# Performance work log

Measured on AMD Instinct MI355X. Metric: run time of the kernel, lower is better.

## Reference

```python
import jax, jax.numpy as jnp
import numpy as np

THETA = 10000.0
BLOCK_SIZE = 8192  # max_cache_len; T >= BLOCK_SIZE triggers eviction
NEG_INF = -1e30


def _rope_cos_sin(head_dim, seq_len, dtype):
    inv_freq = 1.0 / (THETA ** (jnp.arange(0, head_dim, 2, dtype=jnp.float32) / head_dim))
    freqs = jnp.arange(seq_len, dtype=jnp.float32)[:, None] * inv_freq[None, :]  # (T, hd/2)
    return jnp.cos(freqs).astype(dtype), jnp.sin(freqs).astype(dtype)


def _apply_rope(x, cos, sin):
    # x: (B, T, hd); complex multiply on interleaved pairs, matching torch.view_as_complex
    B, T, hd = x.shape
    xr = x.reshape(B, T, hd // 2, 2)
    x0, x1 = xr[..., 0], xr[..., 1]
    out = jnp.stack([x0 * cos - x1 * sin, x0 * sin + x1 * cos], axis=-1)
    return out.reshape(B, T, hd)


def setup_inputs() -> dict:
    key = jax.random.key(0)
    kx, kk, kq, kv = jax.random.split(key, 4)
    B, T, C, hd = 1, 8192, 1024, 64
    x = jax.random.normal(kx, (B, T, C), dtype=jnp.float32)
    Wk = 0.02 * jax.random.normal(kk, (C, hd), dtype=jnp.float32)
    Wq = 0.02 * jax.random.normal(kq, (C, hd), dtype=jnp.float32)
    Wv = 0.02 * jax.random.normal(kv, (C, hd), dtype=jnp.float32)
    return {"x": x, "Wk": Wk, "Wq": Wq, "Wv": Wv}


def reference(x, Wk, Wq, Wv):
    # Warm-up branch of Head.forward: RoPE QK causal attention + importance-based eviction.
    B, T, C = x.shape
    hd = Wk.shape[1]
    k = x @ Wk  # (B, T, hd)
    q = x @ Wq
    v = x @ Wv
    cos, sin = _rope_cos_sin(hd, T, x.dtype)
    k = _apply_rope(k, cos, sin)
    q = _apply_rope(q, cos, sin)
    scale = hd ** -0.5
    scores = jnp.einsum('btd,bsd->bts', q, k) * scale  # (B, T, T)
    causal = jnp.tril(jnp.ones((T, T), dtype=bool))
    scores = jnp.where(causal[None], scores, NEG_INF)
    wei = jax.nn.softmax(scores, axis=-1)
    out = jnp.einsum('bts,bsd->btd', wei, v)  # (B, T, hd)
    # importance-based KV-cache eviction (T >= BLOCK_SIZE here)
    col_sums = wei.sum(axis=1)  # (B, T)
    evict_id = jnp.argmin(col_sums.reshape(-1))  # flattened argmin, as torch.argmin (B=1)
    keep = jnp.arange(T - 1)
    keep = keep + (keep >= evict_id)  # all indices except evict_id
    importance = jnp.take(wei, keep, axis=1)  # evict row in dim 1: (B, T-1, T)
    cache_k = jnp.take(k, keep, axis=1)       # (B, T-1, hd)
    cache_v = jnp.take(v, keep, axis=1)       # (B, T-1, hd)
    return out, importance, cache_k, cache_v
```

## Files before the change

kernel.cpp:

```cpp
#include <hip/hip_runtime.h>

#define TT 8192
#define CC 1024
#define HD 64
#define TAIL0 (TT - 64)
#define IMP_OFF ((size_t)TT * HD)
#define CK_OFF (IMP_OFF + (size_t)(TT - 1) * TT)
#define CV_OFF (CK_OFF + (size_t)(TT - 1) * HD)

typedef float f32x4 __attribute__((ext_vector_type(4)));
typedef short short8 __attribute__((ext_vector_type(8)));

static __device__ __forceinline__ short f2bf(float f) {
  union { float f; unsigned u; } v; v.f = f;
  unsigned u = v.u;
  unsigned r = (u + 0x7fffu + ((u >> 16) & 1u)) >> 16;
  return (short)r;
}
static __device__ __forceinline__ float bf2f(short h) {
  union { unsigned u; float f; } v;
  v.u = ((unsigned)(unsigned short)h) << 16;
  return v.f;
}
static __device__ __forceinline__ f32x4 mfma16(short8 a, short8 b, f32x4 c) {
  return __builtin_amdgcn_mfma_f32_16x16x32_bf16(a, b, c, 0, 0, 0);
}

__global__ void prep(const float* __restrict__ Wk, const float* __restrict__ Wq,
                     const float* __restrict__ Wv, short* __restrict__ wth,
                     short* __restrict__ wtl, float* __restrict__ colsums,
                     float* __restrict__ ctab, float* __restrict__ stab) {
  const int b = blockIdx.x;
  if (b < 768) {
    const int tid = b * 256 + threadIdx.x;
    const int col = tid >> 10, c = tid & 1023;
    const int m = col >> 6, d = col & 63;
    const float* W = (m == 0) ? Wk : (m == 1) ? Wq : Wv;
    const float w = W[c * HD + d];
    const short h = f2bf(w);
    wth[col * CC + c] = h;
    wtl[col * CC + c] = f2bf(w - bf2f(h));
  } else if (b < 800) {
    const int t = (b - 768) * 256 + threadIdx.x;
    colsums[t] = 0.0f;
  } else {
    const int t = (b - 800) * 256 + threadIdx.x;
    const int row = t >> 5, fi = t & 31;
    const float inv = (float)(1.0 / pow(10000.0, (double)fi / 32.0));
    const float ang = (float)row * inv;
    float sn, cs;
    sincosf(ang, &sn, &cs);
    ctab[t] = cs; stab[t] = sn;
  }
}

__global__ __launch_bounds__(256) void qkv_rope(
    const float* __restrict__ x, const short* __restrict__ wth,
    const short* __restrict__ wtl, const float* __restrict__ ctab,
    const float* __restrict__ stab,
    short* __restrict__ qb, short* __restrict__ kb, short* __restrict__ vt,
    float* __restrict__ kf, float* __restrict__ vf, float* __restrict__ qf) {
  __shared__ short xsh[16][1024];
  __shared__ short xsl[16][1024];
  const int tid = threadIdx.x;
  const int lane = tid & 63, wv = tid >> 6;
  const int g = lane >> 4, lr = lane & 15, g8 = g * 8;
  const int r0 = blockIdx.x * 16;

  for (int i = tid; i < 16 * 128; i += 256) {
    const int row = i >> 7, u = i & 127;
    const float4 a4 = *(const float4*)&x[(size_t)(r0 + row) * CC + u * 8];
    const float4 b4 = *(const float4*)&x[(size_t)(r0 + row) * CC + u * 8 + 4];
    const float xv[8] = {a4.x, a4.y, a4.z, a4.w, b4.x, b4.y, b4.z, b4.w};
    short8 h, l;
#pragma unroll
    for (int t = 0; t < 8; ++t) {
      h[t] = f2bf(xv[t]);
      l[t] = f2bf(xv[t] - bf2f(h[t]));
    }
    const int us = (u ^ (row & 7)) * 8;
    *(short8*)&xsh[row][us] = h;
    *(short8*)&xsl[row][us] = l;
  }
  __syncthreads();

  const int ct0 = wv * 3;
  f32x4 acc[3];
#pragma unroll
  for (int i = 0; i < 3; ++i) acc[i] = (f32x4){0.f, 0.f, 0.f, 0.f};
  for (int kc = 0; kc < 32; ++kc) {
    const int us = ((kc * 4 + g) ^ (lr & 7)) * 8;
    const short8 ah = *(const short8*)&xsh[lr][us];
    const short8 al = *(const short8*)&xsl[lr][us];
    const int k0 = kc * 32 + g8;
#pragma unroll
    for (int t = 0; t < 3; ++t) {
      const int ct = ct0 + t;
      const short8 bh = *(const short8*)&wth[(ct * 16 + lr) * CC + k0];
      const short8 bl = *(const short8*)&wtl[(ct * 16 + lr) * CC + k0];
      acc[t] = mfma16(ah, bh, acc[t]);
      acc[t] = mfma16(al, bh, acc[t]);
      acc[t] = mfma16(ah, bl, acc[t]);
    }
  }
#pragma unroll
  for (int t = 0; t < 3; ++t) {
    const int col = ct0 * 16 + t * 16 + lr;
    const int m = col >> 6, d = col & 63;
#pragma unroll
    for (int r = 0; r < 4; ++r) {
      const int row = r0 + g * 4 + r;
      const float val = acc[t][r];
      if (m == 2) {
        vf[row * HD + d] = val;
        vt[(size_t)d * TT + row] = f2bf(val);
      } else {
        const float partner = __shfl_xor(val, 1);
        const int fi = d >> 1;
        const float cs = ctab[row * 32 + fi];
        const float sn = stab[row * 32 + fi];
        const float res = (d & 1) ? (partner * sn + val * cs)
                                  : (val * cs - partner * sn);
        if (m == 0) { kf[row * HD + d] = res; kb[row * HD + d] = f2bf(res); }
        else        { qf[row * HD + d] = res; qb[row * HD + d] = f2bf(res); }
      }
    }
  }
}

__global__ __launch_bounds__(512) void attn_row(
    const short* __restrict__ qb, const short* __restrict__ kb,
    const short* __restrict__ vt, float* __restrict__ colsums,
    float* __restrict__ outp, float* __restrict__ stash,
    float* __restrict__ linv_g) {
  const int tid = threadIdx.x;
  const int lane = tid & 63, wv = tid >> 6;
  const int g = lane >> 4, lr = lane & 15, g8 = g * 8;
  const int bid = (int)blockIdx.x;
  const int rt = (bid < 256) ? (511 - bid) : (bid - 256);
  const int r0 = rt * 16, rmax = r0 + 15;
  const int nkt = rt + 1;
  const int nktp = (nkt + 1) >> 1;
  float* imp = outp + IMP_OFF;
  const float4 z4 = (float4){0.f, 0.f, 0.f, 0.f};

  __shared__ float et[8][16][36];
  __shared__ float l4[8][16];

  const short8 a0 = *(const short8*)&qb[(r0 + lr) * HD + g8];
  const short8 a1 = *(const short8*)&qb[(r0 + lr) * HD + 32 + g8];

  float lacc[4] = {0.f, 0.f, 0.f, 0.f};
  for (int kt = wv; kt < nkt; kt += 8) {
    const int j0 = kt * 16;
    const short8 b0 = *(const short8*)&kb[(j0 + lr) * HD + g8];
    const short8 b1 = *(const short8*)&kb[(j0 + lr) * HD + 32 + g8];
    f32x4 sv = (f32x4){0.f, 0.f, 0.f, 0.f};
    sv = mfma16(a0, b0, sv);
    sv = mfma16(a1, b1, sv);
    const int j = j0 + lr;
#pragma unroll
    for (int r = 0; r < 4; ++r) {
      const int i = r0 + g * 4 + r;
      if (j <= i) lacc[r] += __expf(sv[r] * 0.125f);
    }
  }
#pragma unroll
  for (int r = 0; r < 4; ++r) {
#pragma unroll
    for (int m = 1; m < 16; m <<= 1) lacc[r] += __shfl_xor(lacc[r], m);
  }
  if (lr == 0) {
#pragma unroll
    for (int r = 0; r < 4; ++r) l4[wv][g * 4 + r] = lacc[r];
  }
  __syncthreads();
  float rinv[4];
#pragma unroll
  for (int r = 0; r < 4; ++r) {
    const int row = g * 4 + r;
    float s = 0.f;
#pragma unroll
    for (int w = 0; w < 8; ++w) s += l4[w][row];
    rinv[r] = 1.0f / s;
  }
  if (wv == 0 && lr == 0) {
#pragma unroll
    for (int r = 0; r < 4; ++r) linv_g[r0 + g * 4 + r] = rinv[r];
  }

  f32x4 oacc[4];
#pragma unroll
  for (int ct = 0; ct < 4; ++ct) oacc[ct] = (f32x4){0.f, 0.f, 0.f, 0.f};
  const int worow = lane >> 3, wof4 = (lane & 7) * 4;
  for (int kp = wv; kp < nktp; kp += 8) {
    const int j0p = kp * 32;
#pragma unroll
    for (int h = 0; h < 2; ++h) {
      const int j0 = j0p + h * 16;
      float w4[4] = {0.f, 0.f, 0.f, 0.f};
      if (j0 <= rmax) {
        const short8 b0 = *(const short8*)&kb[(j0 + lr) * HD + g8];
        const short8 b1 = *(const short8*)&kb[(j0 + lr) * HD + 32 + g8];
        f32x4 sv = (f32x4){0.f, 0.f, 0.f, 0.f};
        sv = mfma16(a0, b0, sv);
        sv = mfma16(a1, b1, sv);
        const int j = j0 + lr;
#pragma unroll
        for (int r = 0; r < 4; ++r) {
          const int i = r0 + g * 4 + r;
          w4[r] = (j <= i) ? __expf(sv[r] * 0.125f) * rinv[r] : 0.0f;
        }
        float csum = w4[0] + w4[1] + w4[2] + w4[3];
        csum += __shfl_xor(csum, 16);
        csum += __shfl_xor(csum, 32);
        if (lane < 16 && csum > 0.f) atomicAdd(&colsums[j0 + lane], csum);
      }
#pragma unroll
      for (int r = 0; r < 4; ++r) et[wv][g * 4 + r][h * 16 + lr] = w4[r];
    }
    const float4 e0 = *(const float4*)&et[wv][lr][g8];
    const float4 e1 = *(const float4*)&et[wv][lr][g8 + 4];
    short8 ea;
    ea[0] = f2bf(e0.x); ea[1] = f2bf(e0.y); ea[2] = f2bf(e0.z); ea[3] = f2bf(e0.w);
    ea[4] = f2bf(e1.x); ea[5] = f2bf(e1.y); ea[6] = f2bf(e1.z); ea[7] = f2bf(e1.w);
#pragma unroll
    for (int ct = 0; ct < 4; ++ct) {
      const short8 bv = *(const short8*)&vt[(size_t)(ct * 16 + lr) * TT + j0p + g8];
      oacc[ct] = mfma16(ea, bv, oacc[ct]);
    }
#pragma unroll
    for (int p = 0; p < 2; ++p) {
      const int row = p * 8 + worow;
      const int i = r0 + row;
      const float4 v = *(const float4*)&et[wv][row][wof4];
      if (i < TT - 1) *(float4*)&imp[(size_t)i * TT + j0p + wof4] = v;
      else            *(float4*)&stash[j0p + wof4] = v;
    }
  }
  const int zstart = nktp * 32;
  for (int row = 0; row < 16; ++row) {
    const int i = r0 + row;
    float* dst = (i < TT - 1) ? &imp[(size_t)i * TT] : stash;
    for (int c = zstart + tid * 4; c < TT; c += 2048) *(float4*)&dst[c] = z4;
  }
  __syncthreads();
  float* cbuf = &et[0][0][0];
#pragma unroll
  for (int step = 4; step >= 1; step >>= 1) {
    if (wv >= step && wv < 2 * step) {
      float* dst = cbuf + (size_t)(wv - step) * 1024;
#pragma unroll
      for (int ct = 0; ct < 4; ++ct)
#pragma unroll
        for (int r = 0; r < 4; ++r)
          dst[(g * 4 + r) * 64 + ct * 16 + lr] = oacc[ct][r];
    }
    __syncthreads();
    if (wv < step) {
      const float* src = cbuf + (size_t)wv * 1024;
#pragma unroll
      for (int ct = 0; ct < 4; ++ct)
#pragma unroll
        for (int r = 0; r < 4; ++r)
          oacc[ct][r] += src[(g * 4 + r) * 64 + ct * 16 + lr];
    }
    __syncthreads();
  }
  if (wv == 0) {
#pragma unroll
    for (int ct = 0; ct < 4; ++ct)
#pragma unroll
      for (int r = 0; r < 4; ++r)
        outp[(size_t)(r0 + g * 4 + r) * HD + ct * 16 + lr] = oacc[ct][r];
  }
}

__global__ __launch_bounds__(256) void tail_exact(
    const float* __restrict__ qf, const float* __restrict__ kf,
    float* __restrict__ l_exact, float* __restrict__ tail_e) {
  const int b = blockIdx.x;
  const int i = TAIL0 + b;
  const int tid = threadIdx.x;
  __shared__ float qs[64];
  __shared__ float ws4[4];
  if (tid < 64) {
    qs[tid] = qf[i * HD + tid];
    if (TAIL0 + tid > i) tail_e[(b << 6) + tid] = 0.0f;
  }
  __syncthreads();
  float part = 0.f;
  for (int j = tid; j <= i; j += 256) {
    const float* kr = &kf[(size_t)j * HD];
    float dot = 0.f;
#pragma unroll
    for (int d = 0; d < 64; ++d) dot += qs[d] * kr[d];
    const float e = expf(dot * 0.125f);
    part += e;
    if (j >= TAIL0) tail_e[(b << 6) + (j - TAIL0)] = e;
  }
#pragma unroll
  for (int m = 1; m < 64; m <<= 1) part += __shfl_xor(part, m);
  if ((tid & 63) == 0) ws4[tid >> 6] = part;
  __syncthreads();
  if (tid == 0) l_exact[b] = ws4[0] + ws4[1] + ws4[2] + ws4[3];
}

__global__ void argmin_k(const float* __restrict__ colsums,
                         const float* __restrict__ l_exact,
                         const float* __restrict__ tail_e,
                         int* __restrict__ evict) {
  __shared__ float sv[4];
  __shared__ int si[4];
  const int tid = threadIdx.x, lane = tid & 63, wv = tid >> 6;
  float best = 3.4e38f; int bi = TT;
  for (int j = tid; j < TT; j += 256) {
    float v;
    if (j >= TAIL0) {
      const int jc = j - TAIL0;
      v = 0.f;
      for (int b = jc; b < 64; ++b) v += tail_e[(b << 6) + jc] / l_exact[b];
    } else {
      v = colsums[j];
    }
    if (v < best) { best = v; bi = j; }
  }
#pragma unroll
  for (int m = 1; m < 64; m <<= 1) {
    const float ov = __shfl_xor(best, m);
    const int oi = __shfl_xor(bi, m);
    if (ov < best || (ov == best && oi < bi)) { best = ov; bi = oi; }
  }
  if (lane == 0) { sv[wv] = best; si[wv] = bi; }
  __syncthreads();
  if (tid == 0) {
    for (int w = 1; w < 4; ++w)
      if (sv[w] < best || (sv[w] == best && si[w] < bi)) { best = sv[w]; bi = si[w]; }
    evict[0] = bi;
  }
}

__global__ __launch_bounds__(256) void fix_cache(
    const float* __restrict__ qf, const float* __restrict__ kf,
    const float* __restrict__ vf, const float* __restrict__ linv,
    const float* __restrict__ stash, const int* __restrict__ evict,
    float* __restrict__ outp) {
  const int bid = (int)blockIdx.x;
  const int tid = threadIdx.x;
  const int eid = evict[0];
  if (bid < 512) {
    float* imp = outp + IMP_OFF;
    __shared__ float qs[64];
    for (int dst = eid + bid; dst < TT - 1; dst += 512) {
      const int src = dst + 1;
      if (src == TT - 1) {
        for (int c = tid; c < TT / 4; c += 256)
          ((float4*)&imp[(size_t)dst * TT])[c] = ((const float4*)stash)[c];
      } else {
        if (tid < 64) qs[tid] = qf[src * HD + tid];
        __syncthreads();
        const float rinv = linv[src];
        for (int j = tid; j < TT; j += 256) {
          float w = 0.f;
          if (j <= src) {
            const float* kr = &kf[(size_t)j * HD];
            float dot = 0.f;
#pragma unroll
            for (int d = 0; d < 64; ++d) dot += qs[d] * kr[d];
            w = expf(dot * 0.125f) * rinv;
          }
          imp[(size_t)dst * TT + j] = w;
        }
        __syncthreads();
      }
    }
  } else {
    const int t = (bid - 512) * 256 + tid;
    const int per = (TT - 1) * (HD / 4);
    if (t >= 2 * per) return;
    const int m = t / per;
    const int rem = t - m * per;
    const int r = rem >> 4, c4 = rem & 15;
    const int src = r + (r >= eid);
    const float* sp = m ? vf : kf;
    const float4 val = *(const float4*)&sp[src * HD + c4 * 4];
    float* dst = outp + (m ? CV_OFF : CK_OFF);
    *(float4*)&dst[r * HD + c4 * 4] = val;
  }
}

extern "C" void kernel_launch(void* const* d_in, const int* in_sizes, int n_in,
                              void* d_out, int out_size, void* d_ws, size_t ws_size,
                              hipStream_t stream) {
  const float* x  = (const float*)d_in[0];
  const float* Wk = (const float*)d_in[1];
  const float* Wq = (const float*)d_in[2];
  const float* Wv = (const float*)d_in[3];
  float* outp = (float*)d_out;
  char* ws = (char*)d_ws;
  short* qb      = (short*)(ws);
  short* kb      = (short*)(ws + (1u << 20));
  short* vt      = (short*)(ws + (2u << 20));
  float* kf      = (float*)(ws + (3u << 20));
  float* vf      = (float*)(ws + (5u << 20));
  float* qf      = (float*)(ws + (7u << 20));
  float* linv    = (float*)(ws + (9u << 20));
  int*   evict   = (int*)  (ws + (9u << 20) + (64u << 10));
  float* colsums = (float*)(ws + (9u << 20) + (384u << 10));
  short* wth     = (short*)(ws + (9u << 20) + (448u << 10));
  short* wtl     = (short*)(ws + (9u << 20) + (832u << 10));
  float* tail_e  = (float*)(ws + (9u << 20) + (1280u << 10));
  float* l_exact = (float*)(ws + (9u << 20) + (1344u << 10));
  float* stash   = (float*)(ws + (9u << 20) + (1408u << 10));
  float* ctab    = (float*)(ws + (12u << 20));
  float* stab    = (float*)(ws + (13u << 20));

  prep<<<1824, 256, 0, stream>>>(Wk, Wq, Wv, wth, wtl, colsums, ctab, stab);
  qkv_rope<<<512, 256, 0, stream>>>(x, wth, wtl, ctab, stab, qb, kb, vt, kf, vf, qf);
  attn_row<<<512, 512, 0, stream>>>(qb, kb, vt, colsums, outp, stash, linv);
  tail_exact<<<64, 256, 0, stream>>>(qf, kf, l_exact, tail_e);
  argmin_k<<<1, 256, 0, stream>>>(colsums, l_exact, tail_e, evict);
  fix_cache<<<1536, 256, 0, stream>>>(qf, kf, vf, linv, stash, evict, outp);
}
```

Baseline: 280.4 us.

## Unroll attention loops by two tiles and use nontemporal stores for importance output

The row-sum and weight/PV loops in attn_row now process two key tiles per iteration. Loads for both are issued up front, and the second tile goes into separate LDS staging and accumulators, so more memory-level parallelism hides load latency. The large importance matrix writes, the zero fill, and the cache copies switch to nontemporal stores to avoid polluting cache with write-once data. The cost is extra LDS (a second staging buffer) and higher register pressure, which may reduce occupancy.

Result: faster. 264.2 us (-5.8%).

```diff
diff --git a/kernel.cpp b/kernel.cpp
--- a/kernel.cpp
+++ b/kernel.cpp
@@ -24,6 +24,9 @@
 }
 static __device__ __forceinline__ f32x4 mfma16(short8 a, short8 b, f32x4 c) {
   return __builtin_amdgcn_mfma_f32_16x16x32_bf16(a, b, c, 0, 0, 0);
+}
+static __device__ __forceinline__ void nt_store4(float* p, f32x4 v) {
+  __builtin_nontemporal_store(v, (f32x4*)p);
 }
 
 __global__ void prep(const float* __restrict__ Wk, const float* __restrict__ Wq,
@@ -142,27 +145,41 @@
   const int nkt = rt + 1;
   const int nktp = (nkt + 1) >> 1;
   float* imp = outp + IMP_OFF;
-  const float4 z4 = (float4){0.f, 0.f, 0.f, 0.f};
+  const f32x4 z4 = (f32x4){0.f, 0.f, 0.f, 0.f};
 
   __shared__ float et[8][16][36];
+  __shared__ float et2[8][16][36];
   __shared__ float l4[8][16];
 
   const short8 a0 = *(const short8*)&qb[(r0 + lr) * HD + g8];
   const short8 a1 = *(const short8*)&qb[(r0 + lr) * HD + 32 + g8];
 
   float lacc[4] = {0.f, 0.f, 0.f, 0.f};
-  for (int kt = wv; kt < nkt; kt += 8) {
-    const int j0 = kt * 16;
-    const short8 b0 = *(const short8*)&kb[(j0 + lr) * HD + g8];
-    const short8 b1 = *(const short8*)&kb[(j0 + lr) * HD + 32 + g8];
-    f32x4 sv = (f32x4){0.f, 0.f, 0.f, 0.f};
-    sv = mfma16(a0, b0, sv);
-    sv = mfma16(a1, b1, sv);
-    const int j = j0 + lr;
+  for (int kt = wv; kt < nkt; kt += 16) {
+    const int ktb = kt + 8;
+    const bool has1 = (ktb < nkt);
+    const int j00 = kt * 16, j01 = ktb * 16;
+    const short8 b00 = *(const short8*)&kb[(j00 + lr) * HD + g8];
+    const short8 b01 = *(const short8*)&kb[(j00 + lr) * HD + 32 + g8];
+    short8 b10, b11;
+    if (has1) {
+      b10 = *(const short8*)&kb[(j01 + lr) * HD + g8];
+      b11 = *(const short8*)&kb[(j01 + lr) * HD + 32 + g8];
+    }
+    f32x4 sv0 = z4;
+    sv0 = mfma16(a0, b00, sv0);
+    sv0 = mfma16(a1, b01, sv0);
+    f32x4 sv1 = z4;
+    if (has1) {
+      sv1 = mfma16(a0, b10, sv1);
+      sv1 = mfma16(a1, b11, sv1);
+    }
+    const int jj0 = j00 + lr, jj1 = j01 + lr;
 #pragma unroll
     for (int r = 0; r < 4; ++r) {
       const int i = r0 + g * 4 + r;
-      if (j <= i) lacc[r] += __expf(sv[r] * 0.125f);
+      if (jj0 <= i) lacc[r] += __expf(sv0[r] * 0.125f);
+      if (has1 && jj1 <= i) lacc[r] += __expf(sv1[r] * 0.125f);
     }
   }
 #pragma unroll
@@ -189,61 +206,99 @@
     for (int r = 0; r < 4; ++r) linv_g[r0 + g * 4 + r] = rinv[r];
   }
 
-  f32x4 oacc[4];
-#pragma unroll
-  for (int ct = 0; ct < 4; ++ct) oacc[ct] = (f32x4){0.f, 0.f, 0.f, 0.f};
+  f32x4 oacc[4], oacc2[4];
+#pragma unroll
+  for (int ct = 0; ct < 4; ++ct) { oacc[ct] = z4; oacc2[ct] = z4; }
   const int worow = lane >> 3, wof4 = (lane & 7) * 4;
-  for (int kp = wv; kp < nktp; kp += 8) {
-    const int j0p = kp * 32;
-#pragma unroll
-    for (int h = 0; h < 2; ++h) {
-      const int j0 = j0p + h * 16;
-      float w4[4] = {0.f, 0.f, 0.f, 0.f};
-      if (j0 <= rmax) {
-        const short8 b0 = *(const short8*)&kb[(j0 + lr) * HD + g8];
-        const short8 b1 = *(const short8*)&kb[(j0 + lr) * HD + 32 + g8];
-        f32x4 sv = (f32x4){0.f, 0.f, 0.f, 0.f};
-        sv = mfma16(a0, b0, sv);
-        sv = mfma16(a1, b1, sv);
-        const int j = j0 + lr;
-#pragma unroll
-        for (int r = 0; r < 4; ++r) {
-          const int i = r0 + g * 4 + r;
-          w4[r] = (j <= i) ? __expf(sv[r] * 0.125f) * rinv[r] : 0.0f;
+  for (int kp = wv; kp < nktp; kp += 16) {
+    const int kpb = kp + 8;
+    const bool has1 = (kpb < nktp);
+    const int j0p0 = kp * 32, j0p1 = kpb * 32;
+    short8 bv0[4], bv1[4];
+#pragma unroll
+    for (int ct = 0; ct < 4; ++ct)
+      bv0[ct] = *(const short8*)&vt[(size_t)(ct * 16 + lr) * TT + j0p0 + g8];
+    if (has1) {
+#pragma unroll
+      for (int ct = 0; ct < 4; ++ct)
+        bv1[ct] = *(const short8*)&vt[(size_t)(ct * 16 + lr) * TT + j0p1 + g8];
+    }
+#pragma unroll
+    for (int c = 0; c < 2; ++c) {
+      if (c == 1 && !has1) break;
+      const int j0p = c ? j0p1 : j0p0;
+      float (*etp)[36] = c ? et2[wv] : et[wv];
+#pragma unroll
+      for (int h = 0; h < 2; ++h) {
+        const int j0 = j0p + h * 16;
+        float w4[4] = {0.f, 0.f, 0.f, 0.f};
+        if (j0 <= rmax) {
+          const short8 b0 = *(const short8*)&kb[(j0 + lr) * HD + g8];
+          const short8 b1 = *(const short8*)&kb[(j0 + lr) * HD + 32 + g8];
+          f32x4 sv = z4;
+          sv = mfma16(a0, b0, sv);
+          sv = mfma16(a1, b1, sv);
+          const int j = j0 + lr;
+#pragma unroll
+          for (int r = 0; r < 4; ++r) {
+            const int i = r0 + g * 4 + r;
+            w4[r] = (j <= i) ? __expf(sv[r] * 0.125f) * rinv[r] : 0.0f;
+          }
+          float csum = w4[0] + w4[1] + w4[2] + w4[3];
+          csum += __shfl_xor(csum, 16);
+          csum += __shfl_xor(csum, 32);
+          if (lane < 16 && csum > 0.f) atomicAdd(&colsums[j0 + lane], csum);
         }
-        float csum = w4[0] + w4[1] + w4[2] + w4[3];
-        csum += __shfl_xor(csum, 16);
-        csum += __shfl_xor(csum, 32);
-        if (lane < 16 && csum > 0.f) atomicAdd(&colsums[j0 + lane], csum);
+#pragma unroll
+        for (int r = 0; r < 4; ++r) etp[g * 4 + r][h * 16 + lr] = w4[r];
       }
-#pragma unroll
-      for (int r = 0; r < 4; ++r) et[wv][g * 4 + r][h * 16 + lr] = w4[r];
-    }
-    const float4 e0 = *(const float4*)&et[wv][lr][g8];
-    const float4 e1 = *(const float4*)&et[wv][lr][g8 + 4];
-    short8 ea;
-    ea[0] = f2bf(e0.x); ea[1] = f2bf(e0.y); ea[2] = f2bf(e0.z); ea[3] = f2bf(e0.w);
-    ea[4] = f2bf(e1.x); ea[5] = f2bf(e1.y); ea[6] = f2bf(e1.z); ea[7] = f2bf(e1.w);
-#pragma unroll
-    for (int ct = 0; ct < 4; ++ct) {
-      const short8 bv = *(const short8*)&vt[(size_t)(ct * 16 + lr) * TT + j0p + g8];
-      oacc[ct] = mfma16(ea, bv, oacc[ct]);
+    }
+    {
+      const float4 e0 = *(const float4*)&et[wv][lr][g8];
+      const float4 e1 = *(const float4*)&et[wv][lr][g8 + 4];
+      short8 ea;
+      ea[0] = f2bf(e0.x); ea[1] = f2bf(e0.y); ea[2] = f2bf(e0.z); ea[3] = f2bf(e0.w);
+      ea[4] = f2bf(e1.x); ea[5] = f2bf(e1.y); ea[6] = f2bf(e1.z); ea[7] = f2bf(e1.w);
+#pragma unroll
+      for (int ct = 0; ct < 4; ++ct) oacc[ct] = mfma16(ea, bv0[ct], oacc[ct]);
+    }
+    if (has1) {
+      const float4 e0 = *(const float4*)&et2[wv][lr][g8];
+      const float4 e1 = *(const float4*)&et2[wv][lr][g8 + 4];
+      short8 ea;
+      ea[0] = f2bf(e0.x); ea[1] = f2bf(e0.y); ea[2] = f2bf(e0.z); ea[3] = f2bf(e0.w);
+      ea[4] = f2bf(e1.x); ea[5] = f2bf(e1.y); ea[6] = f2bf(e1.z); ea[7] = f2bf(e1.w);
+#pragma unroll
+      for (int ct = 0; ct < 4; ++ct) oacc2[ct] = mfma16(ea, bv1[ct], oacc2[ct]);
     }
 #pragma unroll
     for (int p = 0; p < 2; ++p) {
       const int row = p * 8 + worow;
       const int i = r0 + row;
-      const float4 v = *(const float4*)&et[wv][row][wof4];
-      if (i < TT - 1) *(float4*)&imp[(size_t)i * TT + j0p + wof4] = v;
-      else            *(float4*)&stash[j0p + wof4] = v;
+      const f32x4 v0 = *(const f32x4*)&et[wv][row][wof4];
+      if (i < TT - 1) nt_store4(&imp[(size_t)i * TT + j0p0 + wof4], v0);
+      else            *(f32x4*)&stash[j0p0 + wof4] = v0;
+      if (has1) {
+        const f32x4 v1 = *(const f32x4*)&et2[wv][row][wof4];
+        if (i < TT - 1) nt_store4(&imp[(size_t)i * TT + j0p1 + wof4], v1);
+        else            *(f32x4*)&stash[j0p1 + wof4] = v1;
+      }
     }
   }
   const int zstart = nktp * 32;
   for (int row = 0; row < 16; ++row) {
     const int i = r0 + row;
-    float* dst = (i < TT - 1) ? &imp[(size_t)i * TT] : stash;
-    for (int c = zstart + tid * 4; c < TT; c += 2048) *(float4*)&dst[c] = z4;
-  }
+    if (i < TT - 1) {
+      float* dst = &imp[(size_t)i * TT];
+      for (int c = zstart + tid * 4; c < TT; c += 2048) nt_store4(&dst[c], z4);
+    } else {
+      for (int c = zstart + tid * 4; c < TT; c += 2048) *(f32x4*)&stash[c] = z4;
+    }
+  }
+#pragma unroll
+  for (int ct = 0; ct < 4; ++ct)
+#pragma unroll
+    for (int r = 0; r < 4; ++r) oacc[ct][r] += oacc2[ct][r];
   __syncthreads();
   float* cbuf = &et[0][0][0];
 #pragma unroll
@@ -355,7 +410,7 @@
       const int src = dst + 1;
       if (src == TT - 1) {
         for (int c = tid; c < TT / 4; c += 256)
-          ((float4*)&imp[(size_t)dst * TT])[c] = ((const float4*)stash)[c];
+          ((f32x4*)&imp[(size_t)dst * TT])[c] = ((const f32x4*)stash)[c];
       } else {
         if (tid < 64) qs[tid] = qf[src * HD + tid];
         __syncthreads();
@@ -383,9 +438,9 @@
     const int r = rem >> 4, c4 = rem & 15;
     const int src = r + (r >= eid);
     const float* sp = m ? vf : kf;
-    const float4 val = *(const float4*)&sp[src * HD + c4 * 4];
+    const f32x4 val = *(const f32x4*)&sp[src * HD + c4 * 4];
     float* dst = outp + (m ? CV_OFF : CK_OFF);
-    *(float4*)&dst[r * HD + c4 * 4] = val;
+    nt_store4(&dst[r * HD + c4 * 4], val);
   }
 }
 
```

## Split attention into separate row-sum pass and two-way key-split weight pass

Applied to the files above, without the earlier changes.

Moves the softmax denominator computation out of the attention kernel into its own pass, parallelised over key chunks with single-wave blocks, plus a small reduction kernel that writes the inverse sums. The main attention kernel is then launched with a second grid dimension that splits the key range in two, accumulating the output rows with atomics into a buffer now zeroed in prep. The huge importance-matrix writes and the cache copies switch to nontemporal stores, and V-tile loads are hoisted ahead of the score MFMAs. This buys more parallelism and lower cache pollution at the cost of extra launches, recomputing QK scores twice, and atomic output accumulation.

After: 300.6 us. 1.07x slower.

```diff
diff --git a/kernel.cpp b/kernel.cpp
--- a/kernel.cpp
+++ b/kernel.cpp
@@ -25,11 +25,15 @@
 static __device__ __forceinline__ f32x4 mfma16(short8 a, short8 b, f32x4 c) {
   return __builtin_amdgcn_mfma_f32_16x16x32_bf16(a, b, c, 0, 0, 0);
 }
+static __device__ __forceinline__ void nt_store4(float* p, f32x4 v) {
+  __builtin_nontemporal_store(v, (f32x4*)p);
+}
 
 __global__ void prep(const float* __restrict__ Wk, const float* __restrict__ Wq,
                      const float* __restrict__ Wv, short* __restrict__ wth,
                      short* __restrict__ wtl, float* __restrict__ colsums,
-                     float* __restrict__ ctab, float* __restrict__ stab) {
+                     float* __restrict__ ctab, float* __restrict__ stab,
+                     float* __restrict__ outp) {
   const int b = blockIdx.x;
   if (b < 768) {
     const int tid = b * 256 + threadIdx.x;
@@ -43,7 +47,7 @@
   } else if (b < 800) {
     const int t = (b - 768) * 256 + threadIdx.x;
     colsums[t] = 0.0f;
-  } else {
+  } else if (b < 1824) {
     const int t = (b - 800) * 256 + threadIdx.x;
     const int row = t >> 5, fi = t & 31;
     const float inv = (float)(1.0 / pow(10000.0, (double)fi / 32.0));
@@ -51,6 +55,9 @@
     float sn, cs;
     sincosf(ang, &sn, &cs);
     ctab[t] = cs; stab[t] = sn;
+  } else {
+    const int t = (b - 1824) * 256 + threadIdx.x;
+    outp[t] = 0.0f;
   }
 }
 
@@ -128,31 +135,22 @@
   }
 }
 
-__global__ __launch_bounds__(512) void attn_row(
+__global__ __launch_bounds__(64) void lpass(
     const short* __restrict__ qb, const short* __restrict__ kb,
-    const short* __restrict__ vt, float* __restrict__ colsums,
-    float* __restrict__ outp, float* __restrict__ stash,
-    float* __restrict__ linv_g) {
-  const int tid = threadIdx.x;
-  const int lane = tid & 63, wv = tid >> 6;
+    float* __restrict__ l_part) {
+  const int lane = threadIdx.x & 63;
   const int g = lane >> 4, lr = lane & 15, g8 = g * 8;
-  const int bid = (int)blockIdx.x;
-  const int rt = (bid < 256) ? (511 - bid) : (bid - 256);
-  const int r0 = rt * 16, rmax = r0 + 15;
-  const int nkt = rt + 1;
-  const int nktp = (nkt + 1) >> 1;
-  float* imp = outp + IMP_OFF;
-  const float4 z4 = (float4){0.f, 0.f, 0.f, 0.f};
-
-  __shared__ float et[8][16][36];
-  __shared__ float l4[8][16];
-
+  const int rt = (int)gridDim.x - 1 - (int)blockIdx.x;
+  const int cc = blockIdx.y;
+  const int r0 = rt * 16, rmax = r0 + 15, c0 = cc * 1024;
+  float* lp = l_part + (size_t)cc * TT;
+  if (c0 > rmax) { if (lane < 16) lp[r0 + lane] = 0.0f; return; }
   const short8 a0 = *(const short8*)&qb[(r0 + lr) * HD + g8];
   const short8 a1 = *(const short8*)&qb[(r0 + lr) * HD + 32 + g8];
-
   float lacc[4] = {0.f, 0.f, 0.f, 0.f};
-  for (int kt = wv; kt < nkt; kt += 8) {
-    const int j0 = kt * 16;
+  const int nkt = min(64, (rmax - c0) / 16 + 1);
+  for (int kt = 0; kt < nkt; ++kt) {
+    const int j0 = c0 + kt * 16;
     const short8 b0 = *(const short8*)&kb[(j0 + lr) * HD + g8];
     const short8 b1 = *(const short8*)&kb[(j0 + lr) * HD + 32 + g8];
     f32x4 sv = (f32x4){0.f, 0.f, 0.f, 0.f};
@@ -172,29 +170,54 @@
   }
   if (lr == 0) {
 #pragma unroll
-    for (int r = 0; r < 4; ++r) l4[wv][g * 4 + r] = lacc[r];
-  }
-  __syncthreads();
+    for (int r = 0; r < 4; ++r) lp[r0 + g * 4 + r] = lacc[r];
+  }
+}
+
+__global__ void linv_k(const float* __restrict__ l_part, float* __restrict__ linv) {
+  const int i = blockIdx.x * 256 + threadIdx.x;
+  if (i >= TT) return;
+  float s = 0.f;
+#pragma unroll
+  for (int cc = 0; cc < 8; ++cc) s += l_part[(size_t)cc * TT + i];
+  linv[i] = 1.0f / s;
+}
+
+__global__ __launch_bounds__(512) void attn_b(
+    const short* __restrict__ qb, const short* __restrict__ kb,
+    const short* __restrict__ vt, const float* __restrict__ linv,
+    float* __restrict__ colsums, float* __restrict__ outp,
+    float* __restrict__ stash) {
+  const int tid = threadIdx.x;
+  const int lane = tid & 63, wv = tid >> 6;
+  const int g = lane >> 4, lr = lane & 15, g8 = g * 8;
+  const int bid = (int)blockIdx.x;
+  const int h2 = (int)blockIdx.y;
+  const int rt = (bid < 256) ? (511 - bid) : (bid - 256);
+  const int r0 = rt * 16, rmax = r0 + 15;
+  const int nkt = rt + 1;
+  const int nktp = (nkt + 1) >> 1;
+  float* imp = outp + IMP_OFF;
+  const f32x4 z4 = (f32x4){0.f, 0.f, 0.f, 0.f};
+
+  __shared__ float et[8][16][36];
+
+  const short8 a0 = *(const short8*)&qb[(r0 + lr) * HD + g8];
+  const short8 a1 = *(const short8*)&qb[(r0 + lr) * HD + 32 + g8];
   float rinv[4];
 #pragma unroll
-  for (int r = 0; r < 4; ++r) {
-    const int row = g * 4 + r;
-    float s = 0.f;
-#pragma unroll
-    for (int w = 0; w < 8; ++w) s += l4[w][row];
-    rinv[r] = 1.0f / s;
-  }
-  if (wv == 0 && lr == 0) {
-#pragma unroll
-    for (int r = 0; r < 4; ++r) linv_g[r0 + g * 4 + r] = rinv[r];
-  }
+  for (int r = 0; r < 4; ++r) rinv[r] = linv[r0 + g * 4 + r];
 
   f32x4 oacc[4];
 #pragma unroll
-  for (int ct = 0; ct < 4; ++ct) oacc[ct] = (f32x4){0.f, 0.f, 0.f, 0.f};
+  for (int ct = 0; ct < 4; ++ct) oacc[ct] = z4;
   const int worow = lane >> 3, wof4 = (lane & 7) * 4;
-  for (int kp = wv; kp < nktp; kp += 8) {
+  for (int kp = wv + 8 * h2; kp < nktp; kp += 16) {
     const int j0p = kp * 32;
+    short8 bv[4];
+#pragma unroll
+    for (int ct = 0; ct < 4; ++ct)
+      bv[ct] = *(const short8*)&vt[(size_t)(ct * 16 + lr) * TT + j0p + g8];
 #pragma unroll
     for (int h = 0; h < 2; ++h) {
       const int j0 = j0p + h * 16;
@@ -202,7 +225,7 @@
       if (j0 <= rmax) {
         const short8 b0 = *(const short8*)&kb[(j0 + lr) * HD + g8];
         const short8 b1 = *(const short8*)&kb[(j0 + lr) * HD + 32 + g8];
-        f32x4 sv = (f32x4){0.f, 0.f, 0.f, 0.f};
+        f32x4 sv = z4;
         sv = mfma16(a0, b0, sv);
         sv = mfma16(a1, b1, sv);
         const int j = j0 + lr;
@@ -225,24 +248,27 @@
     ea[0] = f2bf(e0.x); ea[1] = f2bf(e0.y); ea[2] = f2bf(e0.z); ea[3] = f2bf(e0.w);
     ea[4] = f2bf(e1.x); ea[5] = f2bf(e1.y); ea[6] = f2bf(e1.z); ea[7] = f2bf(e1.w);
 #pragma unroll
-    for (int ct = 0; ct < 4; ++ct) {
-      const short8 bv = *(const short8*)&vt[(size_t)(ct * 16 + lr) * TT + j0p + g8];
-      oacc[ct] = mfma16(ea, bv, oacc[ct]);
-    }
+    for (int ct = 0; ct < 4; ++ct) oacc[ct] = mfma16(ea, bv[ct], oacc[ct]);
 #pragma unroll
     for (int p = 0; p < 2; ++p) {
       const int row = p * 8 + worow;
       const int i = r0 + row;
-      const float4 v = *(const float4*)&et[wv][row][wof4];
-      if (i < TT - 1) *(float4*)&imp[(size_t)i * TT + j0p + wof4] = v;
-      else            *(float4*)&stash[j0p + wof4] = v;
+      const f32x4 v = *(const f32x4*)&et[wv][row][wof4];
+      if (i < TT - 1) nt_store4(&imp[(size_t)i * TT + j0p + wof4], v);
+      else            *(f32x4*)&stash[j0p + wof4] = v;
     }
   }
   const int zstart = nktp * 32;
   for (int row = 0; row < 16; ++row) {
     const int i = r0 + row;
-    float* dst = (i < TT - 1) ? &imp[(size_t)i * TT] : stash;
-    for (int c = zstart + tid * 4; c < TT; c += 2048) *(float4*)&dst[c] = z4;
+    if (i < TT - 1) {
+      float* dst = &imp[(size_t)i * TT];
+      for (int c = zstart + (tid + h2 * 512) * 4; c < TT; c += 4096)
+        nt_store4(&dst[c], z4);
+    } else {
+      for (int c = zstart + (tid + h2 * 512) * 4; c < TT; c += 4096)
+        *(f32x4*)&stash[c] = z4;
+    }
   }
   __syncthreads();
   float* cbuf = &et[0][0][0];
@@ -272,7 +298,7 @@
     for (int ct = 0; ct < 4; ++ct)
 #pragma unroll
       for (int r = 0; r < 4; ++r)
-        outp[(size_t)(r0 + g * 4 + r) * HD + ct * 16 + lr] = oacc[ct][r];
+        atomicAdd(&outp[(size_t)(r0 + g * 4 + r) * HD + ct * 16 + lr], oacc[ct][r]);
   }
 }
 
@@ -355,7 +381,7 @@
       const int src = dst + 1;
       if (src == TT - 1) {
         for (int c = tid; c < TT / 4; c += 256)
-          ((float4*)&imp[(size_t)dst * TT])[c] = ((const float4*)stash)[c];
+          ((f32x4*)&imp[(size_t)dst * TT])[c] = ((const f32x4*)stash)[c];
       } else {
         if (tid < 64) qs[tid] = qf[src * HD + tid];
         __syncthreads();
@@ -383,9 +409,9 @@
     const int r = rem >> 4, c4 = rem & 15;
     const int src = r + (r >= eid);
     const float* sp = m ? vf : kf;
-    const float4 val = *(const float4*)&sp[src * HD + c4 * 4];
+    const f32x4 val = *(const f32x4*)&sp[src * HD + c4 * 4];
     float* dst = outp + (m ? CV_OFF : CK_OFF);
-    *(float4*)&dst[r * HD + c4 * 4] = val;
+    nt_store4(&dst[r * HD + c4 * 4], val);
   }
 }
 
@@ -406,6 +432,7 @@
   float* qf      = (float*)(ws + (7u << 20));
   float* linv    = (float*)(ws + (9u << 20));
   int*   evict   = (int*)  (ws + (9u << 20) + (64u << 10));
+  float* l_part  = (float*)(ws + (9u << 20) + (128u << 10));
   float* colsums = (float*)(ws + (9u << 20) + (384u << 10));
   short* wth     = (short*)(ws + (9u << 20) + (448u << 10));
   short* wtl     = (short*)(ws + (9u << 20) + (832u << 10));
@@ -415,9 +442,11 @@
   float* ctab    = (float*)(ws + (12u << 20));
   float* stab    = (float*)(ws + (13u << 20));
 
-  prep<<<1824, 256, 0, stream>>>(Wk, Wq, Wv, wth, wtl, colsums, ctab, stab);
+  prep<<<3872, 256, 0, stream>>>(Wk, Wq, Wv, wth, wtl, colsums, ctab, stab, outp);
   qkv_rope<<<512, 256, 0, stream>>>(x, wth, wtl, ctab, stab, qb, kb, vt, kf, vf, qf);
-  attn_row<<<512, 512, 0, stream>>>(qb, kb, vt, colsums, outp, stash, linv);
+  lpass<<<dim3(512, 8), 64, 0, stream>>>(qb, kb, l_part);
+  linv_k<<<32, 256, 0, stream>>>(l_part, linv);
+  attn_b<<<dim3(512, 2), 512, 0, stream>>>(qb, kb, vt, linv, colsums, outp, stash);
   tail_exact<<<64, 256, 0, stream>>>(qf, kf, l_exact, tail_e);
   argmin_k<<<1, 256, 0, stream>>>(colsums, l_exact, tail_e, evict);
   fix_cache<<<1536, 256, 0, stream>>>(qf, kf, vf, linv, stash, evict, outp);
```

## Pre-swizzle K/V into MFMA fragment layout, double attn waves, nontemporal stores

Applied to the files above, without the earlier changes.

The QKV kernel now writes bf16 K and V in a layout that already matches the MFMA operand fragments, so each lane loads a contiguous short8 instead of doing strided row or transposed loads. The attention kernel grows from 8 to 16 waves per block, with larger shared reduction buffers and a deeper tree reduction. The large importance-matrix stores and the cache copies switch to nontemporal stores to cut cache pollution on the 256MB output write. The cost is more registers and shared memory per block, which may limit occupancy, and a scattered store pattern in qkv_rope.

Measured after the change: 230.3 us. 1.22x faster.

```diff
diff --git a/kernel.cpp b/kernel.cpp
--- a/kernel.cpp
+++ b/kernel.cpp
@@ -24,6 +24,9 @@
 }
 static __device__ __forceinline__ f32x4 mfma16(short8 a, short8 b, f32x4 c) {
   return __builtin_amdgcn_mfma_f32_16x16x32_bf16(a, b, c, 0, 0, 0);
+}
+static __device__ __forceinline__ void nt_store4(float* p, f32x4 v) {
+  __builtin_nontemporal_store(v, (f32x4*)p);
 }
 
 __global__ void prep(const float* __restrict__ Wk, const float* __restrict__ Wq,
@@ -58,7 +61,7 @@
     const float* __restrict__ x, const short* __restrict__ wth,
     const short* __restrict__ wtl, const float* __restrict__ ctab,
     const float* __restrict__ stab,
-    short* __restrict__ qb, short* __restrict__ kb, short* __restrict__ vt,
+    short* __restrict__ qb, short* __restrict__ kbb, short* __restrict__ vbb,
     float* __restrict__ kf, float* __restrict__ vf, float* __restrict__ qf) {
   __shared__ short xsh[16][1024];
   __shared__ short xsl[16][1024];
@@ -113,7 +116,10 @@
       const float val = acc[t][r];
       if (m == 2) {
         vf[row * HD + d] = val;
-        vt[(size_t)d * TT + row] = f2bf(val);
+        const int kp = row >> 5, r32 = row & 31;
+        const int gv = r32 >> 3, tv = r32 & 7;
+        const int ctv = d >> 4, lrv = d & 15;
+        vbb[kp * 2048 + ctv * 512 + gv * 128 + lrv * 8 + tv] = f2bf(val);
       } else {
         const float partner = __shfl_xor(val, 1);
         const int fi = d >> 1;
@@ -121,16 +127,23 @@
         const float sn = stab[row * 32 + fi];
         const float res = (d & 1) ? (partner * sn + val * cs)
                                   : (val * cs - partner * sn);
-        if (m == 0) { kf[row * HD + d] = res; kb[row * HD + d] = f2bf(res); }
-        else        { qf[row * HD + d] = res; qb[row * HD + d] = f2bf(res); }
+        if (m == 0) {
+          kf[row * HD + d] = res;
+          const int kt = row >> 4, lrk = row & 15;
+          const int hh = d >> 5, gk = (d & 31) >> 3, tk = d & 7;
+          kbb[kt * 1024 + hh * 512 + gk * 128 + lrk * 8 + tk] = f2bf(res);
+        } else {
+          qf[row * HD + d] = res;
+          qb[row * HD + d] = f2bf(res);
+        }
       }
     }
   }
 }
 
-__global__ __launch_bounds__(512) void attn_row(
-    const short* __restrict__ qb, const short* __restrict__ kb,
-    const short* __restrict__ vt, float* __restrict__ colsums,
+__global__ __launch_bounds__(1024) void attn_row(
+    const short* __restrict__ qb, const short* __restrict__ kbb,
+    const short* __restrict__ vbb, float* __restrict__ colsums,
     float* __restrict__ outp, float* __restrict__ stash,
     float* __restrict__ linv_g) {
   const int tid = threadIdx.x;
@@ -142,23 +155,23 @@
   const int nkt = rt + 1;
   const int nktp = (nkt + 1) >> 1;
   float* imp = outp + IMP_OFF;
-  const float4 z4 = (float4){0.f, 0.f, 0.f, 0.f};
-
-  __shared__ float et[8][16][36];
-  __shared__ float l4[8][16];
+  const f32x4 z4 = (f32x4){0.f, 0.f, 0.f, 0.f};
+
+  __shared__ float et[16][16][36];
+  __shared__ float l4[16][16];
 
   const short8 a0 = *(const short8*)&qb[(r0 + lr) * HD + g8];
   const short8 a1 = *(const short8*)&qb[(r0 + lr) * HD + 32 + g8];
+  const int ln8 = lane * 8;
 
   float lacc[4] = {0.f, 0.f, 0.f, 0.f};
-  for (int kt = wv; kt < nkt; kt += 8) {
-    const int j0 = kt * 16;
-    const short8 b0 = *(const short8*)&kb[(j0 + lr) * HD + g8];
-    const short8 b1 = *(const short8*)&kb[(j0 + lr) * HD + 32 + g8];
-    f32x4 sv = (f32x4){0.f, 0.f, 0.f, 0.f};
+  for (int kt = wv; kt < nkt; kt += 16) {
+    const short8 b0 = *(const short8*)&kbb[kt * 1024 + ln8];
+    const short8 b1 = *(const short8*)&kbb[kt * 1024 + 512 + ln8];
+    f32x4 sv = z4;
     sv = mfma16(a0, b0, sv);
     sv = mfma16(a1, b1, sv);
-    const int j = j0 + lr;
+    const int j = kt * 16 + lr;
 #pragma unroll
     for (int r = 0; r < 4; ++r) {
       const int i = r0 + g * 4 + r;
@@ -181,7 +194,7 @@
     const int row = g * 4 + r;
     float s = 0.f;
 #pragma unroll
-    for (int w = 0; w < 8; ++w) s += l4[w][row];
+    for (int w = 0; w < 16; ++w) s += l4[w][row];
     rinv[r] = 1.0f / s;
   }
   if (wv == 0 && lr == 0) {
@@ -191,18 +204,23 @@
 
   f32x4 oacc[4];
 #pragma unroll
-  for (int ct = 0; ct < 4; ++ct) oacc[ct] = (f32x4){0.f, 0.f, 0.f, 0.f};
+  for (int ct = 0; ct < 4; ++ct) oacc[ct] = z4;
   const int worow = lane >> 3, wof4 = (lane & 7) * 4;
-  for (int kp = wv; kp < nktp; kp += 8) {
+  for (int kp = wv; kp < nktp; kp += 16) {
     const int j0p = kp * 32;
+    short8 bv[4];
+#pragma unroll
+    for (int ct = 0; ct < 4; ++ct)
+      bv[ct] = *(const short8*)&vbb[kp * 2048 + ct * 512 + ln8];
 #pragma unroll
     for (int h = 0; h < 2; ++h) {
+      const int kt = kp * 2 + h;
       const int j0 = j0p + h * 16;
       float w4[4] = {0.f, 0.f, 0.f, 0.f};
       if (j0 <= rmax) {
-        const short8 b0 = *(const short8*)&kb[(j0 + lr) * HD + g8];
-        const short8 b1 = *(const short8*)&kb[(j0 + lr) * HD + 32 + g8];
-        f32x4 sv = (f32x4){0.f, 0.f, 0.f, 0.f};
+        const short8 b0 = *(const short8*)&kbb[kt * 1024 + ln8];
+        const short8 b1 = *(const short8*)&kbb[kt * 1024 + 512 + ln8];
+        f32x4 sv = z4;
         sv = mfma16(a0, b0, sv);
         sv = mfma16(a1, b1, sv);
         const int j = j0 + lr;
@@ -225,29 +243,30 @@
     ea[0] = f2bf(e0.x); ea[1] = f2bf(e0.y); ea[2] = f2bf(e0.z); ea[3] = f2bf(e0.w);
     ea[4] = f2bf(e1.x); ea[5] = f2bf(e1.y); ea[6] = f2bf(e1.z); ea[7] = f2bf(e1.w);
 #pragma unroll
-    for (int ct = 0; ct < 4; ++ct) {
-      const short8 bv = *(const short8*)&vt[(size_t)(ct * 16 + lr) * TT + j0p + g8];
-      oacc[ct] = mfma16(ea, bv, oacc[ct]);
-    }
+    for (int ct = 0; ct < 4; ++ct) oacc[ct] = mfma16(ea, bv[ct], oacc[ct]);
 #pragma unroll
     for (int p = 0; p < 2; ++p) {
       const int row = p * 8 + worow;
       const int i = r0 + row;
-      const float4 v = *(const float4*)&et[wv][row][wof4];
-      if (i < TT - 1) *(float4*)&imp[(size_t)i * TT + j0p + wof4] = v;
-      else            *(float4*)&stash[j0p + wof4] = v;
+      const f32x4 v = *(const f32x4*)&et[wv][row][wof4];
+      if (i < TT - 1) nt_store4(&imp[(size_t)i * TT + j0p + wof4], v);
+      else            *(f32x4*)&stash[j0p + wof4] = v;
     }
   }
   const int zstart = nktp * 32;
   for (int row = 0; row < 16; ++row) {
     const int i = r0 + row;
-    float* dst = (i < TT - 1) ? &imp[(size_t)i * TT] : stash;
-    for (int c = zstart + tid * 4; c < TT; c += 2048) *(float4*)&dst[c] = z4;
+    if (i < TT - 1) {
+      float* dst = &imp[(size_t)i * TT];
+      for (int c = zstart + tid * 4; c < TT; c += 4096) nt_store4(&dst[c], z4);
+    } else {
+      for (int c = zstart + tid * 4; c < TT; c += 4096) *(f32x4*)&stash[c] = z4;
+    }
   }
   __syncthreads();
   float* cbuf = &et[0][0][0];
 #pragma unroll
-  for (int step = 4; step >= 1; step >>= 1) {
+  for (int step = 8; step >= 1; step >>= 1) {
     if (wv >= step && wv < 2 * step) {
       float* dst = cbuf + (size_t)(wv - step) * 1024;
 #pragma unroll
@@ -355,7 +374,7 @@
       const int src = dst + 1;
       if (src == TT - 1) {
         for (int c = tid; c < TT / 4; c += 256)
-          ((float4*)&imp[(size_t)dst * TT])[c] = ((const float4*)stash)[c];
+          ((f32x4*)&imp[(size_t)dst * TT])[c] = ((const f32x4*)stash)[c];
       } else {
         if (tid < 64) qs[tid] = qf[src * HD + tid];
         __syncthreads();
@@ -383,9 +402,9 @@
     const int r = rem >> 4, c4 = rem & 15;
     const int src = r + (r >= eid);
     const float* sp = m ? vf : kf;
-    const float4 val = *(const float4*)&sp[src * HD + c4 * 4];
+    const f32x4 val = *(const f32x4*)&sp[src * HD + c4 * 4];
     float* dst = outp + (m ? CV_OFF : CK_OFF);
-    *(float4*)&dst[r * HD + c4 * 4] = val;
+    nt_store4(&dst[r * HD + c4 * 4], val);
   }
 }
 
@@ -399,8 +418,8 @@
   float* outp = (float*)d_out;
   char* ws = (char*)d_ws;
   short* qb      = (short*)(ws);
-  short* kb      = (short*)(ws + (1u << 20));
-  short* vt      = (short*)(ws + (2u << 20));
+  short* kbb     = (short*)(ws + (1u << 20));
+  short* vbb     = (short*)(ws + (2u << 20));
   float* kf      = (float*)(ws + (3u << 20));
   float* vf      = (float*)(ws + (5u << 20));
   float* qf      = (float*)(ws + (7u << 20));
@@ -416,8 +435,8 @@
   float* stab    = (float*)(ws + (13u << 20));
 
   prep<<<1824, 256, 0, stream>>>(Wk, Wq, Wv, wth, wtl, colsums, ctab, stab);
-  qkv_rope<<<512, 256, 0, stream>>>(x, wth, wtl, ctab, stab, qb, kb, vt, kf, vf, qf);
-  attn_row<<<512, 512, 0, stream>>>(qb, kb, vt, colsums, outp, stash, linv);
+  qkv_rope<<<512, 256, 0, stream>>>(x, wth, wtl, ctab, stab, qb, kbb, vbb, kf, vf, qf);
+  attn_row<<<512, 1024, 0, stream>>>(qb, kbb, vbb, colsums, outp, stash, linv);
   tail_exact<<<64, 256, 0, stream>>>(qf, kf, l_exact, tail_e);
   argmin_k<<<1, 256, 0, stream>>>(colsums, l_exact, tail_e, evict);
   fix_cache<<<1536, 256, 0, stream>>>(qf, kf, vf, linv, stash, evict, outp);
```
